# Optimization experiments

Hardware: AMD Instinct MI355X
Metric: run time of the kernel (lower is better)

## Reference

```python
import jax, jax.numpy as jnp
import numpy as np

B, T, OBS, ACT, LAT = 64, 256, 512, 32, 64
BS, NB = 8, 8  # block side length, number of blocks (sum of sides == LAT)
PHI_OUT = NB * BS * BS


def setup_inputs() -> dict:
    key = jax.random.key(0)
    ks = jax.random.split(key, 6)
    w = lambda k, shape: jax.random.normal(k, shape, jnp.float32) * 0.05
    return {
        "observations": jax.random.normal(ks[0], (B, T, OBS), jnp.float32),
        "actions": jax.random.normal(ks[1], (B, T - 1, ACT), jnp.float32),
        "W_enc": w(ks[2], (OBS, LAT)),
        "b_enc": jnp.zeros((LAT,), jnp.float32),
        "W_dec": w(ks[3], (LAT, OBS)),
        "b_dec": jnp.zeros((OBS,), jnp.float32),
        "W_phi": w(ks[4], (ACT, PHI_OUT)),
        "b_phi": jnp.zeros((PHI_OUT,), jnp.float32),
    }


def _forward(observations, actions, W_enc, b_enc, W_dec, b_dec, W_phi, b_phi):
    Bb, Tt = observations.shape[:2]
    Ta = actions.shape[1]  # Tt - 1

    # h(o_t): encoder applied to flattened (B*T) observations
    latent_obs = (observations.reshape(Bb * Tt, OBS) @ W_enc + b_enc).reshape(Bb, Tt, LAT)

    # rho(g_t) = matrix_exp(block_diag(phi(g_t))). Since the matrix is exactly
    # block-diagonal (sum of block sides == LAT), expm factorizes per block.
    after_phi = actions.reshape(Bb * Ta, ACT) @ W_phi + b_phi  # (N, NB*BS*BS)
    # each block is reshaped (BS,BS) then transposed, as in the torch code
    blocks = after_phi.reshape(Bb * Ta * NB, BS, BS).transpose(0, 2, 1)
    exp_blocks = jax.vmap(jax.scipy.linalg.expm)(blocks)  # (N*NB, BS, BS)
    exp_blocks = exp_blocks.reshape(Bb * Ta, NB, BS, BS)
    rho = jnp.zeros((Bb * Ta, LAT, LAT), after_phi.dtype)
    for k in range(NB):  # small fixed structural loop over blocks
        rho = rho.at[:, k * BS:(k + 1) * BS, k * BS:(k + 1) * BS].set(exp_blocks[:, k])
    rho = rho.reshape(Bb, Ta, LAT, LAT)

    # sequential recurrence: h_{t} = h_{t-1} @ rho_{t-1} (row-vector times matrix)
    h0 = latent_obs[:, 0]  # (B, LAT)

    def step(h, rho_t):
        h_new = jnp.einsum('bl,blm->bm', h, rho_t)
        return h_new, h_new

    _, hs = jax.lax.scan(step, h0, jnp.swapaxes(rho, 0, 1))  # (Ta, B, LAT)
    predicted_latents = jnp.concatenate([h0[:, None], jnp.swapaxes(hs, 0, 1)], axis=1)  # (B, T, LAT)

    predicted_obs = (predicted_latents.reshape(Bb * Tt, LAT) @ W_dec + b_dec).reshape(Bb, Tt, OBS)
    return latent_obs, rho, predicted_latents, predicted_obs


def reference(observations, actions, W_enc, b_enc, W_dec, b_dec, W_phi, b_phi):
    return _forward(observations, actions, W_enc, b_enc, W_dec, b_dec, W_phi, b_phi)
```

## Files before the change

### kernel.cpp

```cpp
#include <hip/hip_runtime.h>

#define B_    64
#define T_    256
#define TA_   255
#define OBS_  512
#define ACT_  32
#define LAT_  64
#define NB_   8
#define BS_   8
#define PHI_  512
#define BT_   16384
#define BTA_  16320
#define CH_   8
#define NCH_  32

#define RHO_OFF   1048576ULL
#define PL_OFF    67895296ULL
#define POBS_OFF  68943872ULL

__global__ __launch_bounds__(256) void enc_kernel(
    const float* __restrict__ obs, const float* __restrict__ W,
    const float* __restrict__ bias, float* __restrict__ latent)
{
    __shared__ float At[64][68];
    __shared__ float Wt[64][64];
    const int tid = threadIdx.x;
    const int c0 = (tid & 15) * 4;
    const int r0 = (tid >> 4) * 4;
    const int row0 = blockIdx.x * 64;

    float4 pa[4], pw[4];
#pragma unroll
    for (int j = 0; j < 4; ++j) {
        int ft = tid + j * 256;
        int k4 = ft & 15, r = ft >> 4;
        pa[j] = *(const float4*)(obs + (size_t)(row0 + r) * OBS_ + k4 * 4);
        int c4 = ft & 15, kk = ft >> 4;
        pw[j] = *(const float4*)(W + (size_t)kk * LAT_ + c4 * 4);
    }

    float acc[4][4];
    float4 bv = *(const float4*)(bias + c0);
#pragma unroll
    for (int i = 0; i < 4; ++i) {
        acc[i][0] = bv.x; acc[i][1] = bv.y; acc[i][2] = bv.z; acc[i][3] = bv.w;
    }

    for (int kc = 0; kc < OBS_; kc += 64) {
#pragma unroll
        for (int j = 0; j < 4; ++j) {
            int ft = tid + j * 256;
            int k4 = ft & 15, r = ft >> 4;
            At[k4 * 4 + 0][r] = pa[j].x;
            At[k4 * 4 + 1][r] = pa[j].y;
            At[k4 * 4 + 2][r] = pa[j].z;
            At[k4 * 4 + 3][r] = pa[j].w;
            int c4 = ft & 15, kk = ft >> 4;
            *(float4*)(&Wt[kk][c4 * 4]) = pw[j];
        }
        __syncthreads();
        if (kc + 64 < OBS_) {
#pragma unroll
            for (int j = 0; j < 4; ++j) {
                int ft = tid + j * 256;
                int k4 = ft & 15, r = ft >> 4;
                pa[j] = *(const float4*)(obs + (size_t)(row0 + r) * OBS_ + kc + 64 + k4 * 4);
                int c4 = ft & 15, kk = ft >> 4;
                pw[j] = *(const float4*)(W + (size_t)(kc + 64 + kk) * LAT_ + c4 * 4);
            }
        }
#pragma unroll 4
        for (int kk = 0; kk < 64; ++kk) {
            float4 a = *(const float4*)(&At[kk][r0]);
            float4 w = *(const float4*)(&Wt[kk][c0]);
            acc[0][0] = fmaf(a.x, w.x, acc[0][0]); acc[0][1] = fmaf(a.x, w.y, acc[0][1]);
            acc[0][2] = fmaf(a.x, w.z, acc[0][2]); acc[0][3] = fmaf(a.x, w.w, acc[0][3]);
            acc[1][0] = fmaf(a.y, w.x, acc[1][0]); acc[1][1] = fmaf(a.y, w.y, acc[1][1]);
            acc[1][2] = fmaf(a.y, w.z, acc[1][2]); acc[1][3] = fmaf(a.y, w.w, acc[1][3]);
            acc[2][0] = fmaf(a.z, w.x, acc[2][0]); acc[2][1] = fmaf(a.z, w.y, acc[2][1]);
            acc[2][2] = fmaf(a.z, w.z, acc[2][2]); acc[2][3] = fmaf(a.z, w.w, acc[2][3]);
            acc[3][0] = fmaf(a.w, w.x, acc[3][0]); acc[3][1] = fmaf(a.w, w.y, acc[3][1]);
            acc[3][2] = fmaf(a.w, w.z, acc[3][2]); acc[3][3] = fmaf(a.w, w.w, acc[3][3]);
        }
        __syncthreads();
    }
#pragma unroll
    for (int i = 0; i < 4; ++i)
        *(float4*)(latent + (size_t)(row0 + r0 + i) * LAT_ + c0) =
            make_float4(acc[i][0], acc[i][1], acc[i][2], acc[i][3]);
}

__device__ __forceinline__ void mm8(float* __restrict__ D,
                                    const float* __restrict__ X,
                                    const float* __restrict__ Y)
{
#pragma unroll
    for (int r = 0; r < 8; ++r)
#pragma unroll
        for (int c = 0; c < 8; ++c) {
            float s = 0.f;
#pragma unroll
            for (int q = 0; q < 8; ++q) s = fmaf(X[r * 8 + q], Y[q * 8 + c], s);
            D[r * 8 + c] = s;
        }
}

__global__ __launch_bounds__(256, 1) void phi_expm_kernel(
    const float* __restrict__ act, const float* __restrict__ Wp,
    const float* __restrict__ bp, float* __restrict__ out_blocks,
    float* __restrict__ rho, int use_ws)
{
    const int bt = blockIdx.x * 256 + threadIdx.x;
    const int k  = blockIdx.y;
    if (bt >= BTA_) return;

    float A[64];
    {
        const float* bpp = bp + k * 64;
#pragma unroll
        for (int p = 0; p < 64; ++p) A[p] = bpp[p];
    }
    const float4* arow4 = (const float4*)(act + (size_t)bt * ACT_);
    const float* wk = Wp + k * 64;
#pragma unroll
    for (int a4 = 0; a4 < ACT_ / 4; ++a4) {
        float4 av = arow4[a4];
        const float* wr = wk + (size_t)(a4 * 4) * PHI_;
#pragma unroll
        for (int p = 0; p < 64; ++p) A[p] = fmaf(av.x, wr[p], A[p]);
        wr += PHI_;
#pragma unroll
        for (int p = 0; p < 64; ++p) A[p] = fmaf(av.y, wr[p], A[p]);
        wr += PHI_;
#pragma unroll
        for (int p = 0; p < 64; ++p) A[p] = fmaf(av.z, wr[p], A[p]);
        wr += PHI_;
#pragma unroll
        for (int p = 0; p < 64; ++p) A[p] = fmaf(av.w, wr[p], A[p]);
    }

#pragma unroll
    for (int r = 0; r < 8; ++r) {
        A[r * 9] *= 0.125f;
#pragma unroll
        for (int c = r + 1; c < 8; ++c) {
            float t = A[r * 8 + c];
            A[r * 8 + c] = 0.125f * A[c * 8 + r];
            A[c * 8 + r] = 0.125f * t;
        }
    }

    float P[64];
#pragma unroll
    for (int i = 0; i < 64; ++i) P[i] = (1.f / 5040.f) * A[i];
#pragma unroll
    for (int d = 0; d < 8; ++d) P[d * 9] += 1.f / 720.f;

    constexpr float COEF[6] = {1.f/120.f, 1.f/24.f, 1.f/6.f, 0.5f, 1.f, 1.f};
#pragma unroll
    for (int it = 0; it < 6; ++it) {
        const float coef = COEF[it];
#pragma unroll
        for (int r = 0; r < 8; ++r) {
            float t[8];
#pragma unroll
            for (int c = 0; c < 8; ++c) {
                float s = 0.f;
#pragma unroll
                for (int q = 0; q < 8; ++q) s = fmaf(P[r * 8 + q], A[q * 8 + c], s);
                t[c] = s;
            }
#pragma unroll
            for (int c = 0; c < 8; ++c) P[r * 8 + c] = t[c];
            P[r * 9] += coef;
        }
    }

    float T[64];
    mm8(T, P, P);
    mm8(P, T, T);
    mm8(T, P, P);

    if (use_ws) {
        float* dst = out_blocks + ((size_t)bt * NB_ + k) * 64;
#pragma unroll
        for (int i = 0; i < 16; ++i)
            ((float4*)dst)[i] = make_float4(T[4*i], T[4*i+1], T[4*i+2], T[4*i+3]);
    } else {
        float* base = rho + ((size_t)bt * LAT_ + k * BS_) * LAT_ + k * BS_;
#pragma unroll
        for (int r = 0; r < 8; ++r) {
            *(float4*)(base + (size_t)r * LAT_)     = make_float4(T[r*8+0], T[r*8+1], T[r*8+2], T[r*8+3]);
            *(float4*)(base + (size_t)r * LAT_ + 4) = make_float4(T[r*8+4], T[r*8+5], T[r*8+6], T[r*8+7]);
        }
    }
}

__global__ __launch_bounds__(256) void rho_write_kernel(
    const float* __restrict__ blocks, float* __restrict__ rho)
{
    size_t idx = (size_t)blockIdx.x * 256 + threadIdx.x;
    int c4 = (int)(idx & 15);
    size_t rowg = idx >> 4;
    int row = (int)(rowg & 63);
    size_t bt = rowg >> 6;
    int k = row >> 3, r = row & 7;
    float4 v = make_float4(0.f, 0.f, 0.f, 0.f);
    if ((c4 >> 1) == k)
        v = ((const float4*)(blocks + ((bt * 8 + (size_t)k) * 64 + (size_t)r * 8)))[c4 & 1];
    ((float4*)rho)[idx] = v;
}

__global__ __launch_bounds__(256) void zero_kernel(float4* __restrict__ p)
{
    p[(size_t)blockIdx.x * 256 + threadIdx.x] = make_float4(0.f, 0.f, 0.f, 0.f);
}

#define SL_BODY_(I)                                                           \
    {                                                                         \
        const float* mp = src + (size_t)(I) * 512;                            \
        float M[64];                                                          \
        _Pragma("unroll")                                                     \
        for (int q = 0; q < 16; ++q) ((float4*)M)[q] = ((const float4*)mp)[q];\
        _Pragma("unroll")                                                     \
        for (int r = 0; r < 8; ++r) {                                         \
            float tmp[8];                                                     \
            _Pragma("unroll")                                                 \
            for (int c = 0; c < 8; ++c) {                                     \
                float s = 0.f;                                                \
                _Pragma("unroll")                                             \
                for (int q = 0; q < 8; ++q)                                   \
                    s = fmaf(R[r * 8 + q], M[q * 8 + c], s);                  \
                tmp[c] = s;                                                   \
            }                                                                 \
            _Pragma("unroll")                                                 \
            for (int c = 0; c < 8; ++c) R[r * 8 + c] = tmp[c];                \
        }                                                                     \
        float* dp = dst + (size_t)(I) * 512;                                  \
        _Pragma("unroll")                                                     \
        for (int q = 0; q < 16; ++q) ((float4*)dp)[q] = ((const float4*)R)[q];\
    }

__global__ __launch_bounds__(128, 1) void scan_local_kernel(
    const float* __restrict__ eb, float* __restrict__ pfx)
{
    const int tid = blockIdx.x * 128 + threadIdx.x;
    const int k = tid & 7;
    const int j = (tid >> 3) & 31;
    const int b = tid >> 8;
    const int t0 = j * CH_;
    const int cnt = (TA_ - t0 < CH_) ? (TA_ - t0) : CH_;
    const float* src = eb  + ((size_t)(b * TA_ + t0) * 8 + k) * 64;
    float*       dst = pfx + ((size_t)(b * TA_ + t0) * 8 + k) * 64;

    float R[64];
#pragma unroll
    for (int q = 0; q < 16; ++q) ((float4*)R)[q] = ((const float4*)src)[q];
#pragma unroll
    for (int q = 0; q < 16; ++q) ((float4*)dst)[q] = ((const float4*)R)[q];

    if (cnt == CH_) {
#pragma unroll
        for (int i = 1; i < CH_; ++i) SL_BODY_(i);
    } else {
#pragma unroll
        for (int i = 1; i < CH_ - 1; ++i) SL_BODY_(i);
    }
}
#undef SL_BODY_

__global__ __launch_bounds__(64, 1) void scan_chunk_kernel(
    const float* __restrict__ latent, const float* __restrict__ pfx,
    float* __restrict__ gws, float* __restrict__ pl)
{
    const int tid = blockIdx.x * 64 + threadIdx.x;
    const int k = tid & 7, b = tid >> 3;
    float g[8];
    const float* l0 = latent + (size_t)b * T_ * LAT_ + k * 8;
#pragma unroll
    for (int m = 0; m < 8; ++m) g[m] = l0[m];

    float* pl0 = pl + (size_t)b * T_ * LAT_ + k * 8;
    *(float4*)(pl0)     = make_float4(g[0], g[1], g[2], g[3]);
    *(float4*)(pl0 + 4) = make_float4(g[4], g[5], g[6], g[7]);

    float* gp = gws + ((size_t)(b * NCH_) * 8 + k) * 8;
    *(float4*)(gp)     = make_float4(g[0], g[1], g[2], g[3]);
    *(float4*)(gp + 4) = make_float4(g[4], g[5], g[6], g[7]);

    float C[64];
    {
        const float* cp = pfx + ((size_t)(b * TA_ + CH_ - 1) * 8 + k) * 64;
#pragma unroll
        for (int q = 0; q < 16; ++q) ((float4*)C)[q] = ((const float4*)cp)[q];
    }
    for (int j = 1; j < NCH_; ++j) {
        float Cn[64];
        if (j + 1 < NCH_) {
            const float* cp = pfx + ((size_t)(b * TA_ + (j + 1) * CH_ - 1) * 8 + k) * 64;
#pragma unroll
            for (int q = 0; q < 16; ++q) ((float4*)Cn)[q] = ((const float4*)cp)[q];
        }
        float ng[8];
#pragma unroll
        for (int m = 0; m < 8; ++m) {
            float s = 0.f;
#pragma unroll
            for (int l = 0; l < 8; ++l) s = fmaf(g[l], C[l * 8 + m], s);
            ng[m] = s;
        }
#pragma unroll
        for (int m = 0; m < 8; ++m) g[m] = ng[m];
        float* gq = gws + ((size_t)(b * NCH_ + j) * 8 + k) * 8;
        *(float4*)(gq)     = make_float4(g[0], g[1], g[2], g[3]);
        *(float4*)(gq + 4) = make_float4(g[4], g[5], g[6], g[7]);
#pragma unroll
        for (int q = 0; q < 64; ++q) C[q] = Cn[q];
    }
}

__global__ __launch_bounds__(256, 1) void scan_emit_kernel(
    const float* __restrict__ pfx, const float* __restrict__ gws,
    float* __restrict__ pl)
{
    const int tid = blockIdx.x * 256 + threadIdx.x;
    const int k = tid & 7;
    const int bt = tid >> 3;
    const int b = bt / TA_;
    const int t = bt - b * TA_;
    const int j = t >> 3;

    float g[8];
    const float* gp = gws + ((size_t)(b * NCH_ + j) * 8 + k) * 8;
    *(float4*)(g)     = *(const float4*)(gp);
    *(float4*)(g + 4) = *(const float4*)(gp + 4);

    const float* lp = pfx + ((size_t)bt * 8 + k) * 64;
    float L[64];
#pragma unroll
    for (int q = 0; q < 16; ++q) ((float4*)L)[q] = ((const float4*)lp)[q];

    float h[8];
#pragma unroll
    for (int m = 0; m < 8; ++m) {
        float s = 0.f;
#pragma unroll
        for (int l = 0; l < 8; ++l) s = fmaf(g[l], L[l * 8 + m], s);
        h[m] = s;
    }
    float* op = pl + ((size_t)b * T_ + t + 1) * LAT_ + k * 8;
    *(float4*)(op)     = make_float4(h[0], h[1], h[2], h[3]);
    *(float4*)(op + 4) = make_float4(h[4], h[5], h[6], h[7]);
}

__device__ __forceinline__ void load_block8(float* __restrict__ dst,
                                            const float* __restrict__ p, int rs)
{
#pragma unroll
    for (int r = 0; r < 8; ++r) {
        float4 x = *(const float4*)(p + (size_t)r * rs);
        float4 y = *(const float4*)(p + (size_t)r * rs + 4);
        dst[r*8+0] = x.x; dst[r*8+1] = x.y; dst[r*8+2] = x.z; dst[r*8+3] = x.w;
        dst[r*8+4] = y.x; dst[r*8+5] = y.y; dst[r*8+6] = y.z; dst[r*8+7] = y.w;
    }
}

__global__ __launch_bounds__(64) void recur_kernel(
    const float* __restrict__ latent, const float* __restrict__ eb,
    int chainA, int chainB, int ts, int rs, float* __restrict__ pl)
{
    const int tid = blockIdx.x * 64 + threadIdx.x;
    const int b = tid >> 3, k = tid & 7;
    const float* e = eb + (size_t)b * (size_t)chainA + (size_t)k * (size_t)chainB;

    float h[8];
    const float* l0 = latent + (size_t)b * T_ * LAT_ + k * 8;
#pragma unroll
    for (int j = 0; j < 8; ++j) h[j] = l0[j];
    float* plp = pl + (size_t)b * T_ * LAT_ + k * 8;
    *(float4*)(plp)     = make_float4(h[0], h[1], h[2], h[3]);
    *(float4*)(plp + 4) = make_float4(h[4], h[5], h[6], h[7]);

    float eA[64], eB[64];
    load_block8(eA, e, rs);

#define STEP_(EBUF)                                                          \
    {                                                                        \
        float nh[8];                                                         \
        _Pragma("unroll")                                                    \
        for (int c = 0; c < 8; ++c) {                                        \
            float s = 0.f;                                                   \
            _Pragma("unroll")                                                \
            for (int r = 0; r < 8; ++r) s = fmaf(h[r], EBUF[r * 8 + c], s);  \
            nh[c] = s;                                                       \
        }                                                                    \
        plp += LAT_;                                                         \
        *(float4*)(plp)     = make_float4(nh[0], nh[1], nh[2], nh[3]);       \
        *(float4*)(plp + 4) = make_float4(nh[4], nh[5], nh[6], nh[7]);       \
        _Pragma("unroll")                                                    \
        for (int j = 0; j < 8; ++j) h[j] = nh[j];                            \
    }

    for (int t = 0; t < TA_; t += 2) {
        int tn = (t + 1 < TA_) ? t + 1 : TA_ - 1;
        load_block8(eB, e + (size_t)tn * ts, rs);
        STEP_(eA);
        if (t + 1 >= TA_) break;
        int tn2 = (t + 2 < TA_) ? t + 2 : TA_ - 1;
        load_block8(eA, e + (size_t)tn2 * ts, rs);
        STEP_(eB);
    }
#undef STEP_
}

__global__ __launch_bounds__(256) void dec_kernel(
    const float* __restrict__ pl, const float* __restrict__ W,
    const float* __restrict__ bias, float* __restrict__ out)
{
    __shared__ float At[64][68];
    __shared__ float Wt[64][64];
    const int tid = threadIdx.x;
    const int c0 = (tid & 15) * 4;
    const int r0 = (tid >> 4) * 4;
    const int row0 = blockIdx.x * 64;
    const int n0 = blockIdx.y * 64;

#pragma unroll
    for (int j = 0; j < 4; ++j) {
        int ft = tid + j * 256;
        int k4 = ft & 15, r = ft >> 4;
        float4 v = *(const float4*)(pl + (size_t)(row0 + r) * LAT_ + k4 * 4);
        At[k4 * 4 + 0][r] = v.x;
        At[k4 * 4 + 1][r] = v.y;
        At[k4 * 4 + 2][r] = v.z;
        At[k4 * 4 + 3][r] = v.w;
        int c4 = ft & 15, kk = ft >> 4;
        *(float4*)(&Wt[kk][c4 * 4]) =
            *(const float4*)(W + (size_t)kk * OBS_ + n0 + c4 * 4);
    }
    __syncthreads();

    float acc[4][4];
    float4 bv = *(const float4*)(bias + n0 + c0);
#pragma unroll
    for (int i = 0; i < 4; ++i) {
        acc[i][0] = bv.x; acc[i][1] = bv.y; acc[i][2] = bv.z; acc[i][3] = bv.w;
    }
#pragma unroll 4
    for (int kk = 0; kk < 64; ++kk) {
        float4 a = *(const float4*)(&At[kk][r0]);
        float4 w = *(const float4*)(&Wt[kk][c0]);
        acc[0][0] = fmaf(a.x, w.x, acc[0][0]); acc[0][1] = fmaf(a.x, w.y, acc[0][1]);
        acc[0][2] = fmaf(a.x, w.z, acc[0][2]); acc[0][3] = fmaf(a.x, w.w, acc[0][3]);
        acc[1][0] = fmaf(a.y, w.x, acc[1][0]); acc[1][1] = fmaf(a.y, w.y, acc[1][1]);
        acc[1][2] = fmaf(a.y, w.z, acc[1][2]); acc[1][3] = fmaf(a.y, w.w, acc[1][3]);
        acc[2][0] = fmaf(a.z, w.x, acc[2][0]); acc[2][1] = fmaf(a.z, w.y, acc[2][1]);
        acc[2][2] = fmaf(a.z, w.z, acc[2][2]); acc[2][3] = fmaf(a.z, w.w, acc[2][3]);
        acc[3][0] = fmaf(a.w, w.x, acc[3][0]); acc[3][1] = fmaf(a.w, w.y, acc[3][1]);
        acc[3][2] = fmaf(a.w, w.z, acc[3][2]); acc[3][3] = fmaf(a.w, w.w, acc[3][3]);
    }
#pragma unroll
    for (int i = 0; i < 4; ++i)
        *(float4*)(out + (size_t)(row0 + r0 + i) * OBS_ + n0 + c0) =
            make_float4(acc[i][0], acc[i][1], acc[i][2], acc[i][3]);
}

extern "C" void kernel_launch(void* const* d_in, const int* in_sizes, int n_in,
                              void* d_out, int out_size, void* d_ws, size_t ws_size,
                              hipStream_t stream)
{
    const float* obs  = (const float*)d_in[0];
    const float* act  = (const float*)d_in[1];
    const float* Wenc = (const float*)d_in[2];
    const float* benc = (const float*)d_in[3];
    const float* Wdec = (const float*)d_in[4];
    const float* bdec = (const float*)d_in[5];
    const float* Wphi = (const float*)d_in[6];
    const float* bphi = (const float*)d_in[7];

    float* out    = (float*)d_out;
    float* latent = out;
    float* rho    = out + RHO_OFF;
    float* pl     = out + PL_OFF;
    float* pobs   = out + POBS_OFF;

    const size_t eb_elems = (size_t)BTA_ * NB_ * 64;
    const size_t need_ws   = eb_elems * sizeof(float);
    const size_t need_scan = (2 * eb_elems + 512 * NCH_ * 8) * sizeof(float);
    const bool use_ws   = (ws_size >= need_ws);
    const bool use_scan = (ws_size >= need_scan);
    float* eb  = (float*)d_ws;
    float* pfx = eb + eb_elems;
    float* gws = pfx + eb_elems;

    hipLaunchKernelGGL(enc_kernel, dim3(BT_ / 64), dim3(256), 0, stream,
                       obs, Wenc, benc, latent);

    if (!use_ws)
        hipLaunchKernelGGL(zero_kernel, dim3(66846720 / 1024), dim3(256), 0, stream,
                           (float4*)rho);
    hipLaunchKernelGGL(phi_expm_kernel, dim3((BTA_ + 255) / 256, NB_), dim3(256), 0, stream,
                       act, Wphi, bphi, eb, rho, (int)use_ws);

    if (use_scan) {
        hipLaunchKernelGGL(scan_local_kernel, dim3(16384 / 128), dim3(128), 0, stream,
                           eb, pfx);
        hipLaunchKernelGGL(scan_chunk_kernel, dim3(8), dim3(64), 0, stream,
                           latent, pfx, gws, pl);
        hipLaunchKernelGGL(scan_emit_kernel, dim3(BTA_ * NB_ / 256), dim3(256), 0, stream,
                           pfx, gws, pl);
    } else if (use_ws) {
        hipLaunchKernelGGL(recur_kernel, dim3(8), dim3(64), 0, stream,
                           latent, eb, TA_ * 512, 64, 512, 8, pl);
    } else {
        hipLaunchKernelGGL(recur_kernel, dim3(8), dim3(64), 0, stream,
                           latent, rho, TA_ * 4096, BS_ * LAT_ + BS_, 4096, LAT_, pl);
    }

    if (use_ws)
        hipLaunchKernelGGL(rho_write_kernel, dim3(66846720 / 1024), dim3(256), 0, stream,
                           eb, rho);

    hipLaunchKernelGGL(dec_kernel, dim3(BT_ / 64, OBS_ / 64), dim3(256), 0, stream,
                       pl, Wdec, bdec, pobs);
}
```

Before: 497.5 us.

## Write full rho rows with zeros in expm kernel, drop block workspace

The expm kernel now writes each full 64-wide row slice of rho directly, storing its 8x8 block and zero-filling the rest with nontemporal stores. This removes the intermediate block workspace and the separate rho_write pass that read it back. The scan and recurrence kernels now read their blocks strided out of rho instead of from the compact workspace. The scan_local launch also changes from 128 to 64 threads per block. Each expm thread now issues many scattered 16-byte stores, and the scan reads are less contiguous than before.

```diff
diff --git a/kernel.cpp b/kernel.cpp
--- a/kernel.cpp
+++ b/kernel.cpp
@@ -18,6 +18,8 @@
 #define PL_OFF    67895296ULL
 #define POBS_OFF  68943872ULL
 
+typedef float f32x4 __attribute__((ext_vector_type(4)));
+
 __global__ __launch_bounds__(256) void enc_kernel(
     const float* __restrict__ obs, const float* __restrict__ W,
     const float* __restrict__ bias, float* __restrict__ latent)
@@ -107,8 +109,7 @@
 
 __global__ __launch_bounds__(256, 1) void phi_expm_kernel(
     const float* __restrict__ act, const float* __restrict__ Wp,
-    const float* __restrict__ bp, float* __restrict__ out_blocks,
-    float* __restrict__ rho, int use_ws)
+    const float* __restrict__ bp, float* __restrict__ rho)
 {
     const int bt = blockIdx.x * 256 + threadIdx.x;
     const int k  = blockIdx.y;
@@ -181,47 +182,42 @@
     mm8(P, T, T);
     mm8(T, P, P);
 
-    if (use_ws) {
-        float* dst = out_blocks + ((size_t)bt * NB_ + k) * 64;
-#pragma unroll
-        for (int i = 0; i < 16; ++i)
-            ((float4*)dst)[i] = make_float4(T[4*i], T[4*i+1], T[4*i+2], T[4*i+3]);
-    } else {
-        float* base = rho + ((size_t)bt * LAT_ + k * BS_) * LAT_ + k * BS_;
-#pragma unroll
-        for (int r = 0; r < 8; ++r) {
-            *(float4*)(base + (size_t)r * LAT_)     = make_float4(T[r*8+0], T[r*8+1], T[r*8+2], T[r*8+3]);
-            *(float4*)(base + (size_t)r * LAT_ + 4) = make_float4(T[r*8+4], T[r*8+5], T[r*8+6], T[r*8+7]);
-        }
-    }
-}
-
-__global__ __launch_bounds__(256) void rho_write_kernel(
-    const float* __restrict__ blocks, float* __restrict__ rho)
-{
-    size_t idx = (size_t)blockIdx.x * 256 + threadIdx.x;
-    int c4 = (int)(idx & 15);
-    size_t rowg = idx >> 4;
-    int row = (int)(rowg & 63);
-    size_t bt = rowg >> 6;
-    int k = row >> 3, r = row & 7;
-    float4 v = make_float4(0.f, 0.f, 0.f, 0.f);
-    if ((c4 >> 1) == k)
-        v = ((const float4*)(blocks + ((bt * 8 + (size_t)k) * 64 + (size_t)r * 8)))[c4 & 1];
-    ((float4*)rho)[idx] = v;
-}
-
-__global__ __launch_bounds__(256) void zero_kernel(float4* __restrict__ p)
-{
-    p[(size_t)blockIdx.x * 256 + threadIdx.x] = make_float4(0.f, 0.f, 0.f, 0.f);
+    float* base = rho + ((size_t)bt * LAT_ + (size_t)(k * BS_)) * LAT_;
+    const f32x4 z = {0.f, 0.f, 0.f, 0.f};
+#pragma unroll
+    for (int r = 0; r < 8; ++r) {
+        f32x4* rp = (f32x4*)(base + (size_t)r * LAT_);
+#pragma unroll
+        for (int c4 = 0; c4 < 16; ++c4) {
+            if (c4 == 2 * k) {
+                f32x4 v = {T[r*8+0], T[r*8+1], T[r*8+2], T[r*8+3]};
+                rp[c4] = v;
+            } else if (c4 == 2 * k + 1) {
+                f32x4 v = {T[r*8+4], T[r*8+5], T[r*8+6], T[r*8+7]};
+                rp[c4] = v;
+            } else {
+                __builtin_nontemporal_store(z, rp + c4);
+            }
+        }
+    }
+}
+
+__device__ __forceinline__ void load_block8(float* __restrict__ dst,
+                                            const float* __restrict__ p, int rs)
+{
+#pragma unroll
+    for (int r = 0; r < 8; ++r) {
+        float4 x = *(const float4*)(p + (size_t)r * rs);
+        float4 y = *(const float4*)(p + (size_t)r * rs + 4);
+        dst[r*8+0] = x.x; dst[r*8+1] = x.y; dst[r*8+2] = x.z; dst[r*8+3] = x.w;
+        dst[r*8+4] = y.x; dst[r*8+5] = y.y; dst[r*8+6] = y.z; dst[r*8+7] = y.w;
+    }
 }
 
 #define SL_BODY_(I)                                                           \
     {                                                                         \
-        const float* mp = src + (size_t)(I) * 512;                            \
         float M[64];                                                          \
-        _Pragma("unroll")                                                     \
-        for (int q = 0; q < 16; ++q) ((float4*)M)[q] = ((const float4*)mp)[q];\
+        load_block8(M, src + (size_t)(I) * 4096, LAT_);                       \
         _Pragma("unroll")                                                     \
         for (int r = 0; r < 8; ++r) {                                         \
             float tmp[8];                                                     \
@@ -241,21 +237,20 @@
         for (int q = 0; q < 16; ++q) ((float4*)dp)[q] = ((const float4*)R)[q];\
     }
 
-__global__ __launch_bounds__(128, 1) void scan_local_kernel(
-    const float* __restrict__ eb, float* __restrict__ pfx)
-{
-    const int tid = blockIdx.x * 128 + threadIdx.x;
+__global__ __launch_bounds__(64, 1) void scan_local_kernel(
+    const float* __restrict__ rho, float* __restrict__ pfx)
+{
+    const int tid = blockIdx.x * 64 + threadIdx.x;
     const int k = tid & 7;
     const int j = (tid >> 3) & 31;
     const int b = tid >> 8;
     const int t0 = j * CH_;
     const int cnt = (TA_ - t0 < CH_) ? (TA_ - t0) : CH_;
-    const float* src = eb  + ((size_t)(b * TA_ + t0) * 8 + k) * 64;
+    const float* src = rho + (size_t)(b * TA_ + t0) * 4096 + (size_t)k * (BS_ * LAT_ + BS_);
     float*       dst = pfx + ((size_t)(b * TA_ + t0) * 8 + k) * 64;
 
     float R[64];
-#pragma unroll
-    for (int q = 0; q < 16; ++q) ((float4*)R)[q] = ((const float4*)src)[q];
+    load_block8(R, src, LAT_);
 #pragma unroll
     for (int q = 0; q < 16; ++q) ((float4*)dst)[q] = ((const float4*)R)[q];
 
@@ -353,25 +348,13 @@
     *(float4*)(op + 4) = make_float4(h[4], h[5], h[6], h[7]);
 }
 
-__device__ __forceinline__ void load_block8(float* __restrict__ dst,
-                                            const float* __restrict__ p, int rs)
-{
-#pragma unroll
-    for (int r = 0; r < 8; ++r) {
-        float4 x = *(const float4*)(p + (size_t)r * rs);
-        float4 y = *(const float4*)(p + (size_t)r * rs + 4);
-        dst[r*8+0] = x.x; dst[r*8+1] = x.y; dst[r*8+2] = x.z; dst[r*8+3] = x.w;
-        dst[r*8+4] = y.x; dst[r*8+5] = y.y; dst[r*8+6] = y.z; dst[r*8+7] = y.w;
-    }
-}
-
 __global__ __launch_bounds__(64) void recur_kernel(
-    const float* __restrict__ latent, const float* __restrict__ eb,
-    int chainA, int chainB, int ts, int rs, float* __restrict__ pl)
+    const float* __restrict__ latent, const float* __restrict__ rho,
+    float* __restrict__ pl)
 {
     const int tid = blockIdx.x * 64 + threadIdx.x;
     const int b = tid >> 3, k = tid & 7;
-    const float* e = eb + (size_t)b * (size_t)chainA + (size_t)k * (size_t)chainB;
+    const float* e = rho + (size_t)b * ((size_t)TA_ * 4096) + (size_t)k * (BS_ * LAT_ + BS_);
 
     float h[8];
     const float* l0 = latent + (size_t)b * T_ * LAT_ + k * 8;
@@ -382,7 +365,7 @@
     *(float4*)(plp + 4) = make_float4(h[4], h[5], h[6], h[7]);
 
     float eA[64], eB[64];
-    load_block8(eA, e, rs);
+    load_block8(eA, e, LAT_);
 
 #define STEP_(EBUF)                                                          \
     {                                                                        \
@@ -403,11 +386,11 @@
 
     for (int t = 0; t < TA_; t += 2) {
         int tn = (t + 1 < TA_) ? t + 1 : TA_ - 1;
-        load_block8(eB, e + (size_t)tn * ts, rs);
+        load_block8(eB, e + (size_t)tn * 4096, LAT_);
         STEP_(eA);
         if (t + 1 >= TA_) break;
         int tn2 = (t + 2 < TA_) ? t + 2 : TA_ - 1;
-        load_block8(eA, e + (size_t)tn2 * ts, rs);
+        load_block8(eA, e + (size_t)tn2 * 4096, LAT_);
         STEP_(eB);
     }
 #undef STEP_
@@ -484,42 +467,29 @@
     float* pl     = out + PL_OFF;
     float* pobs   = out + POBS_OFF;
 
-    const size_t eb_elems = (size_t)BTA_ * NB_ * 64;
-    const size_t need_ws   = eb_elems * sizeof(float);
-    const size_t need_scan = (2 * eb_elems + 512 * NCH_ * 8) * sizeof(float);
-    const bool use_ws   = (ws_size >= need_ws);
-    const bool use_scan = (ws_size >= need_scan);
-    float* eb  = (float*)d_ws;
-    float* pfx = eb + eb_elems;
-    float* gws = pfx + eb_elems;
+    const size_t pfx_elems = (size_t)BTA_ * NB_ * 64;
+    const size_t gws_elems = 512ULL * NCH_ * 8;
+    const bool use_scan = (ws_size >= (pfx_elems + gws_elems) * sizeof(float));
+    float* pfx = (float*)d_ws;
+    float* gws = pfx + pfx_elems;
 
     hipLaunchKernelGGL(enc_kernel, dim3(BT_ / 64), dim3(256), 0, stream,
                        obs, Wenc, benc, latent);
 
-    if (!use_ws)
-        hipLaunchKernelGGL(zero_kernel, dim3(66846720 / 1024), dim3(256), 0, stream,
-                           (float4*)rho);
     hipLaunchKernelGGL(phi_expm_kernel, dim3((BTA_ + 255) / 256, NB_), dim3(256), 0, stream,
-                       act, Wphi, bphi, eb, rho, (int)use_ws);
+                       act, Wphi, bphi, rho);
 
     if (use_scan) {
-        hipLaunchKernelGGL(scan_local_kernel, dim3(16384 / 128), dim3(128), 0, stream,
-                           eb, pfx);
+        hipLaunchKernelGGL(scan_local_kernel, dim3(16384 / 64), dim3(64), 0, stream,
+                           rho, pfx);
         hipLaunchKernelGGL(scan_chunk_kernel, dim3(8), dim3(64), 0, stream,
                            latent, pfx, gws, pl);
         hipLaunchKernelGGL(scan_emit_kernel, dim3(BTA_ * NB_ / 256), dim3(256), 0, stream,
                            pfx, gws, pl);
-    } else if (use_ws) {
-        hipLaunchKernelGGL(recur_kernel, dim3(8), dim3(64), 0, stream,
-                           latent, eb, TA_ * 512, 64, 512, 8, pl);
     } else {
         hipLaunchKernelGGL(recur_kernel, dim3(8), dim3(64), 0, stream,
-                           latent, rho, TA_ * 4096, BS_ * LAT_ + BS_, 4096, LAT_, pl);
-    }
-
-    if (use_ws)
-        hipLaunchKernelGGL(rho_write_kernel, dim3(66846720 / 1024), dim3(256), 0, stream,
-                           eb, rho);
+                           latent, rho, pl);
+    }
 
     hipLaunchKernelGGL(dec_kernel, dim3(BT_ / 64, OBS_ / 64), dim3(256), 0, stream,
                        pl, Wdec, bdec, pobs);
```

Result: slower. 647.6 us (+30.2%).
